# Optimization experiments

Hardware: AMD Instinct MI355X
Metric: run time of the kernel (lower is better)

The kernel has to match this reference:

```python
import jax, jax.numpy as jnp
import numpy as np

B, S, D = 2, 2048, 2048
H, KV, HD = 32, 8, 64          # n_heads, n_kv_heads, head_dim
REP = H // KV                  # 4
THETA = 10000.0


def _rotate_half(u):
    h = u.shape[-1] // 2
    return jnp.concatenate([-u[..., h:], u[..., :h]], axis=-1)


def setup_inputs() -> dict:
    key = jax.random.key(0)
    ks = jax.random.split(key, 5)
    x = jax.random.normal(ks[0], (B, S, D), dtype=jnp.float32)
    Wq = jax.random.normal(ks[1], (D, H * HD), dtype=jnp.float32) * 0.02
    Wk = jax.random.normal(ks[2], (D, KV * HD), dtype=jnp.float32) * 0.02
    Wv = jax.random.normal(ks[3], (D, KV * HD), dtype=jnp.float32) * 0.02
    Wo = jax.random.normal(ks[4], (H * HD, D), dtype=jnp.float32) * 0.02
    return {"x": x, "Wq": Wq, "Wk": Wk, "Wv": Wv, "Wo": Wo}


def reference(x, Wq, Wk, Wv, Wo):
    b, s, d = x.shape
    # QKV projections (nn.Linear, no bias)
    q = (x @ Wq).reshape(b, s, H, HD).transpose(0, 2, 1, 3)   # [B,H,S,HD]
    k = (x @ Wk).reshape(b, s, KV, HD).transpose(0, 2, 1, 3)  # [B,KV,S,HD]
    v = (x @ Wv).reshape(b, s, KV, HD).transpose(0, 2, 1, 3)  # [B,KV,S,HD]

    # RoPE (position_offset = 0)
    inv_freq = 1.0 / (THETA ** (jnp.arange(0, HD, 2, dtype=jnp.float32) / HD))
    freqs = jnp.outer(jnp.arange(s, dtype=jnp.float32), inv_freq)  # [S,HD/2]
    emb = jnp.concatenate([freqs, freqs], axis=-1)                  # [S,HD]
    cos, sin = jnp.cos(emb), jnp.sin(emb)
    q = q * cos + _rotate_half(q) * sin
    k = k * cos + _rotate_half(k) * sin

    # Grouped attention: avoid materializing repeated KV tensors.
    qg = q.reshape(b, KV, REP, s, HD)                               # [B,KV,REP,S,HD]
    scale = 1.0 / np.sqrt(HD)
    scores = jnp.einsum('bgrqd,bgkd->bgrqk', qg, k) * scale         # [B,KV,REP,S,S]
    causal = jnp.tril(jnp.ones((s, s), dtype=bool))
    scores = jnp.where(causal, scores, jnp.finfo(jnp.float32).min)
    probs = jax.nn.softmax(scores.astype(jnp.float32), axis=-1).astype(q.dtype)
    out = jnp.einsum('bgrqk,bgkd->bgrqd', probs, v)                 # [B,KV,REP,S,HD]
    out = out.reshape(b, H, s, HD).transpose(0, 2, 1, 3).reshape(b, s, H * HD)
    return out @ Wo                                                  # [B,S,D]
```

## Files before the change

kernel.cpp:

```cpp
#include <hip/hip_runtime.h>
#include <math.h>

typedef __bf16 bf16_t;
typedef bf16_t bf16x8 __attribute__((ext_vector_type(8)));
typedef bf16_t bf16x4 __attribute__((ext_vector_type(4)));
typedef float floatx4 __attribute__((ext_vector_type(4)));
typedef short short4v __attribute__((ext_vector_type(4)));

#define MFMA16(a, b, c) __builtin_amdgcn_mfma_f32_16x16x32_bf16((a), (b), (c), 0, 0, 0)

#if __has_builtin(__builtin_amdgcn_exp2f)
#define PEXP(x) __builtin_amdgcn_exp2f(x)
#define SCORE_SCALE (0.125f * 1.4426950408889634f)
#else
#define PEXP(x) __expf(x)
#define SCORE_SCALE 0.125f
#endif

#if __has_builtin(__builtin_amdgcn_mfma_f32_16x16x16bf16_1k)
#define HAVE_MFMA_K16 1
__device__ __forceinline__ floatx4 mfma_k16(bf16x4 a, bf16x4 b, floatx4 c)
{
    union { bf16x4 v; short4v s; } ua, ub;
    ua.v = a; ub.v = b;
    return __builtin_amdgcn_mfma_f32_16x16x16bf16_1k(ua.s, ub.s, c, 0, 0, 0);
}
#endif

union PU { unsigned u[2]; bf16x4 v; };
union BU { unsigned u[4]; bf16x8 v; };

__device__ __forceinline__ void gld16(const void* g, void* lds)
{
    __builtin_amdgcn_global_load_lds(
        reinterpret_cast<const __attribute__((address_space(1))) void*>(
            reinterpret_cast<uintptr_t>(g)),
        reinterpret_cast<__attribute__((address_space(3))) void*>(
            (unsigned int)reinterpret_cast<uintptr_t>(lds)),
        16, 0, 0);
}

template <typename TC>
__device__ __forceinline__ void gemm_bt_body(
    const bf16_t* __restrict__ A, const bf16_t* __restrict__ Bt,
    TC* __restrict__ C, int row0, int col0, int N, int K,
    bf16_t* As, bf16_t* Bs)
{
    const int tid  = threadIdx.x;
    const int wave = tid >> 6, lane = tid & 63;
    const int quad = lane >> 4, l16 = lane & 15;
    const int wm = (wave >> 1) * 64, wn = (wave & 1) * 64;

    floatx4 acc[4][4] = {};

    for (int k0 = 0; k0 < K; k0 += 64) {
        __syncthreads();
        #pragma unroll
        for (int i = 0; i < 4; ++i) {
            int c = i * 256 + tid;
            int r = c >> 3, s = c & 7;
            int ks = k0 + ((s ^ (r & 7)) << 3);
            gld16(A  + (size_t)(row0 + r) * K + ks, &As[(i * 256 + wave * 64) * 8]);
            gld16(Bt + (size_t)(col0 + r) * K + ks, &Bs[(i * 256 + wave * 64) * 8]);
        }
        __syncthreads();
        #pragma unroll
        for (int kh = 0; kh < 2; ++kh) {
            bf16x8 af[4], bfr[4];
            #pragma unroll
            for (int t = 0; t < 4; ++t) {
                int ar = wm + t * 16 + l16;
                af[t]  = *(const bf16x8*)&As[ar * 64 + (((kh * 4 + quad) ^ (ar & 7)) << 3)];
                int br = wn + t * 16 + l16;
                bfr[t] = *(const bf16x8*)&Bs[br * 64 + (((kh * 4 + quad) ^ (br & 7)) << 3)];
            }
            #pragma unroll
            for (int mt = 0; mt < 4; ++mt)
                #pragma unroll
                for (int nt = 0; nt < 4; ++nt)
                    acc[mt][nt] = MFMA16(af[mt], bfr[nt], acc[mt][nt]);
        }
    }
    #pragma unroll
    for (int mt = 0; mt < 4; ++mt)
        #pragma unroll
        for (int nt = 0; nt < 4; ++nt)
            #pragma unroll
            for (int r = 0; r < 4; ++r)
                C[(size_t)(row0 + wm + mt * 16 + quad * 4 + r) * N
                  + col0 + wn + nt * 16 + l16] = (TC)acc[mt][nt][r];
}

template <typename TC>
__global__ __launch_bounds__(256) void gemm_bt(
    const bf16_t* __restrict__ A, const bf16_t* __restrict__ Bt,
    TC* __restrict__ C, int N, int K)
{
    __shared__ bf16_t As[128 * 64];
    __shared__ bf16_t Bs[128 * 64];
    gemm_bt_body<TC>(A, Bt, C, blockIdx.y * 128, blockIdx.x * 128, N, K, As, Bs);
}

__global__ __launch_bounds__(256) void gemm_qkv(
    const bf16_t* __restrict__ A, const bf16_t* __restrict__ BtQ,
    const bf16_t* __restrict__ BtK, const bf16_t* __restrict__ BtV,
    bf16_t* __restrict__ CQ, bf16_t* __restrict__ CK, bf16_t* __restrict__ CV)
{
    __shared__ bf16_t As[128 * 64];
    __shared__ bf16_t Bs[128 * 64];
    const int x = blockIdx.x;
    const bf16_t* Bt; bf16_t* C; int N, col0;
    if (x < 16)      { Bt = BtQ; C = CQ; N = 2048; col0 = x * 128; }
    else if (x < 20) { Bt = BtK; C = CK; N = 512;  col0 = (x - 16) * 128; }
    else             { Bt = BtV; C = CV; N = 512;  col0 = (x - 20) * 128; }
    gemm_bt_body<bf16_t>(A, Bt, C, blockIdx.y * 128, col0, N, 2048, As, Bs);
}

__device__ __forceinline__ void transpose_body(
    const float* __restrict__ W, bf16_t* __restrict__ Wt, int K, int N,
    int bx, int by, float (*t)[33], int tid)
{
    int tx = tid & 31, ty = tid >> 5;
    #pragma unroll
    for (int i = 0; i < 32; i += 8)
        t[ty + i][tx] = W[(size_t)(by + ty + i) * N + bx + tx];
    __syncthreads();
    #pragma unroll
    for (int i = 0; i < 32; i += 8)
        Wt[(size_t)(bx + ty + i) * K + by + tx] = (bf16_t)t[tx][ty + i];
}

__global__ __launch_bounds__(256) void prep_all(
    const float* __restrict__ x, const float* __restrict__ Wq,
    const float* __restrict__ Wk, const float* __restrict__ Wv,
    bf16_t* __restrict__ xb, bf16_t* __restrict__ WqT,
    bf16_t* __restrict__ WkT, bf16_t* __restrict__ WvT)
{
    __shared__ float t[32][33];
    const int blk = blockIdx.x, tid = threadIdx.x;
    if (blk < 8192) {
        int i = blk * 256 + tid;
        float4 f = ((const float4*)x)[i];
        bf16x4 v = {(bf16_t)f.x, (bf16_t)f.y, (bf16_t)f.z, (bf16_t)f.w};
        ((bf16x4*)xb)[i] = v;
    } else if (blk < 12288) {
        int r = blk - 8192;
        transpose_body(Wq, WqT, 2048, 2048, (r & 63) * 32, (r >> 6) * 32, t, tid);
    } else if (blk < 13312) {
        int r = blk - 12288;
        transpose_body(Wk, WkT, 2048, 512, (r & 15) * 32, (r >> 4) * 32, t, tid);
    } else {
        int r = blk - 13312;
        transpose_body(Wv, WvT, 2048, 512, (r & 15) * 32, (r >> 4) * 32, t, tid);
    }
}

__global__ __launch_bounds__(256) void mid_all(
    bf16_t* __restrict__ Kw, const bf16_t* __restrict__ Vw,
    bf16_t* __restrict__ VtG, const float* __restrict__ Wo,
    bf16_t* __restrict__ WoT)
{
    __shared__ float tf[32][33];
    __shared__ bf16_t tb[32][34];
    const int blk = blockIdx.x, tid = threadIdx.x;
    if (blk < 4096) {
        int idx = blk * 256 + tid;
        int i   = idx & 31;
        int h   = (idx >> 5) & 7;
        int row = idx >> 8;
        int pos = row & 2047;
        float invf = powf(10000.0f, -(float)i / 32.0f);
        float sv, cv;
        sincosf((float)pos * invf, &sv, &cv);
        size_t base = (size_t)row * 512 + (size_t)h * 64 + i;
        float a  = (float)Kw[base];
        float b2 = (float)Kw[base + 32];
        Kw[base]      = (bf16_t)(a * cv - b2 * sv);
        Kw[base + 32] = (bf16_t)(b2 * cv + a * sv);
    } else if (blk < 6144) {
        int r  = blk - 4096;
        int bz = r >> 10, r2 = r & 1023;
        int bx = (r2 & 15) * 32, by = (r2 >> 4) * 32;
        int tx = tid & 31, ty = tid >> 5;
        #pragma unroll
        for (int i = 0; i < 32; i += 8)
            tb[ty + i][tx] = Vw[((size_t)bz * 2048 + by + ty + i) * 512 + bx + tx];
        __syncthreads();
        #pragma unroll
        for (int i = 0; i < 32; i += 8)
            VtG[((size_t)bz * 512 + bx + ty + i) * 2048 + by + tx] = tb[tx][ty + i];
    } else {
        int r = blk - 6144;
        transpose_body(Wo, WoT, 2048, 2048, (r & 63) * 32, (r >> 6) * 32, tf, tid);
    }
}

__global__ __launch_bounds__(256) void gqa_attn(
    const bf16_t* __restrict__ Q, const bf16_t* __restrict__ Kc,
    const bf16_t* __restrict__ Vt, bf16_t* __restrict__ AO)
{
    __shared__ alignas(16) bf16_t Ks[2][64 * 64];
    __shared__ alignas(16) bf16_t Vs[2][64 * 64];

    const int x = blockIdx.x, h = blockIdx.y, b = blockIdx.z, g = h >> 2;
    const int tid  = threadIdx.x;
    const int wave = tid >> 6, lane = tid & 63;
    const int quad = lane >> 4, l16 = lane & 15;

    #pragma unroll 1
    for (int t = 0; t < 2; ++t) {
        const int qt = t ? x : (15 - x);
        const int q0 = qt * 128;
        int qb[2];
        qb[0] = q0 + wave * 16;
        qb[1] = qb[0] + 64;

        bf16x8 qf[2][2];
        #pragma unroll
        for (int mt = 0; mt < 2; ++mt) {
            int qrow = qb[mt] + l16;
            const bf16_t* qp = Q + (size_t)(b * 2048 + qrow) * 2048 + h * 64 + quad * 8;
            bf16x8 lo = *(const bf16x8*)qp;
            bf16x8 hi = *(const bf16x8*)(qp + 32);
            #pragma unroll
            for (int j = 0; j < 8; ++j) {
                int d = quad * 8 + j;
                float invf = powf(10000.0f, -(float)d / 32.0f);
                float sv, cv;
                sincosf((float)qrow * invf, &sv, &cv);
                float a = (float)lo[j], c2 = (float)hi[j];
                qf[mt][0][j] = (bf16_t)((a * cv - c2 * sv) * SCORE_SCALE);
                qf[mt][1][j] = (bf16_t)((c2 * cv + a * sv) * SCORE_SCALE);
            }
        }

        floatx4 o[2][4] = {};
        floatx4 ls4[2] = {};

        const int ktmax = 2 * qt + 1;

        __asm__ volatile("s_waitcnt lgkmcnt(0)" ::: "memory");
        __builtin_amdgcn_s_barrier();
        #pragma unroll
        for (int i = 0; i < 2; ++i) {
            int c = i * 256 + tid;
            int r = c >> 3, s = c & 7;
            int sw = (s ^ (r & 7)) << 3;
            gld16(Kc + (size_t)(b * 2048 + r) * 512 + g * 64 + sw,
                  &Ks[0][(i * 256 + wave * 64) * 8]);
            gld16(Vt + (size_t)(b * 512 + g * 64 + r) * 2048 + sw,
                  &Vs[0][(i * 256 + wave * 64) * 8]);
        }

        #pragma unroll 1
        for (int kt = 0; kt <= ktmax; ++kt) {
            const int cur = kt & 1;
            if (kt < ktmax) {
                const int kn = kt + 1;
                #pragma unroll
                for (int i = 0; i < 2; ++i) {
                    int c = i * 256 + tid;
                    int r = c >> 3, s = c & 7;
                    int sw = (s ^ (r & 7)) << 3;
                    gld16(Kc + (size_t)(b * 2048 + kn * 64 + r) * 512 + g * 64 + sw,
                          &Ks[cur ^ 1][(i * 256 + wave * 64) * 8]);
                    gld16(Vt + (size_t)(b * 512 + g * 64 + r) * 2048 + kn * 64 + sw,
                          &Vs[cur ^ 1][(i * 256 + wave * 64) * 8]);
                }
                __asm__ volatile("s_waitcnt vmcnt(4)" ::: "memory");
            } else {
                __asm__ volatile("s_waitcnt vmcnt(0)" ::: "memory");
            }
            __builtin_amdgcn_s_barrier();

            bool en[2];
            en[0] = (kt * 64) <= (qb[0] + 15);
            en[1] = (kt * 64) <= (qb[1] + 15);

            floatx4 st[2][4] = {};
            #pragma unroll
            for (int nt = 0; nt < 4; ++nt) {
                int kr = nt * 16 + l16;
                bf16x8 kf0 = *(const bf16x8*)&Ks[cur][kr * 64 + ((quad ^ (kr & 7)) << 3)];
                bf16x8 kf1 = *(const bf16x8*)&Ks[cur][kr * 64 + (((4 + quad) ^ (kr & 7)) << 3)];
                if (en[0]) {
                    st[0][nt] = MFMA16(kf0, qf[0][0], st[0][nt]);
                    st[0][nt] = MFMA16(kf1, qf[0][1], st[0][nt]);
                }
                if (en[1]) {
                    st[1][nt] = MFMA16(kf0, qf[1][0], st[1][nt]);
                    st[1][nt] = MFMA16(kf1, qf[1][1], st[1][nt]);
                }
            }

            PU pk[2][4];
            #pragma unroll
            for (int mt = 0; mt < 2; ++mt) {
                if (!en[mt]) continue;
                const bool diag = (kt * 64 + 63) > qb[mt];
                const int qa = qb[mt] + l16;
                #pragma unroll
                for (int nt = 0; nt < 4; ++nt) {
                    float pv[4];
                    #pragma unroll
                    for (int r = 0; r < 4; ++r) {
                        float e = PEXP(st[mt][nt][r]);
                        if (diag) {
                            int ka = kt * 64 + nt * 16 + quad * 4 + r;
                            if (ka > qa) e = 0.f;
                        }
                        ls4[mt][r] += e;
                        pv[r] = e;
                    }
                    pk[mt][nt].v = bf16x4{(bf16_t)pv[0], (bf16_t)pv[1],
                                          (bf16_t)pv[2], (bf16_t)pv[3]};
                }
            }

#ifdef HAVE_MFMA_K16
            #pragma unroll
            for (int nt = 0; nt < 4; ++nt)
                #pragma unroll
                for (int dt = 0; dt < 4; ++dt) {
                    int vr = dt * 16 + l16;
                    int slot = ((nt << 1) | (quad >> 1)) ^ (vr & 7);
                    bf16x4 va = *(const bf16x4*)&Vs[cur][vr * 64 + (slot << 3)
                                                         + ((quad & 1) << 2)];
                    if (en[0]) o[0][dt] = mfma_k16(va, pk[0][nt].v, o[0][dt]);
                    if (en[1]) o[1][dt] = mfma_k16(va, pk[1][nt].v, o[1][dt]);
                }
#else
            #pragma unroll
            for (int H = 0; H < 2; ++H) {
                BU bfv[2];
                #pragma unroll
                for (int mt = 0; mt < 2; ++mt) {
                    if (!en[mt]) continue;
                    #pragma unroll
                    for (int j = 0; j < 4; ++j) {
                        int srcl = (((quad & 1) << 1) + (j >> 1)) * 16 + l16;
                        unsigned a0 = (unsigned)__shfl((int)pk[mt][2 * H].u[j & 1], srcl, 64);
                        unsigned a1 = (unsigned)__shfl((int)pk[mt][2 * H + 1].u[j & 1], srcl, 64);
                        bfv[mt].u[j] = (quad >> 1) ? a1 : a0;
                    }
                }
                #pragma unroll
                for (int dt = 0; dt < 4; ++dt) {
                    int vr = dt * 16 + l16;
                    bf16x8 va = *(const bf16x8*)&Vs[cur][vr * 64
                                  + ((((H << 2) | quad) ^ (vr & 7)) << 3)];
                    if (en[0]) o[0][dt] = MFMA16(va, bfv[0].v, o[0][dt]);
                    if (en[1]) o[1][dt] = MFMA16(va, bfv[1].v, o[1][dt]);
                }
            }
#endif
            __asm__ volatile("s_waitcnt lgkmcnt(0)" ::: "memory");
            __builtin_amdgcn_s_barrier();
        }

        #pragma unroll
        for (int mt = 0; mt < 2; ++mt) {
            float l = ls4[mt][0] + ls4[mt][1] + ls4[mt][2] + ls4[mt][3];
            l += __shfl_xor(l, 16, 64);
            l += __shfl_xor(l, 32, 64);
            float rc = 1.0f / l;
            #pragma unroll
            for (int dt = 0; dt < 4; ++dt) {
                bf16x4 ov = {(bf16_t)(o[mt][dt][0] * rc), (bf16_t)(o[mt][dt][1] * rc),
                             (bf16_t)(o[mt][dt][2] * rc), (bf16_t)(o[mt][dt][3] * rc)};
                *(bf16x4*)&AO[(size_t)(b * 2048 + qb[mt] + l16) * 2048
                              + h * 64 + dt * 16 + quad * 4] = ov;
            }
        }
    }
}

extern "C" void kernel_launch(void* const* d_in, const int* in_sizes, int n_in,
                              void* d_out, int out_size, void* d_ws, size_t ws_size,
                              hipStream_t stream)
{
    const float* x  = (const float*)d_in[0];
    const float* Wq = (const float*)d_in[1];
    const float* Wk = (const float*)d_in[2];
    const float* Wv = (const float*)d_in[3];
    const float* Wo = (const float*)d_in[4];
    float* out = (float*)d_out;

    const size_t MB = 1024 * 1024;
    char* ws = (char*)d_ws;
    bf16_t* xb_AO = (bf16_t*)(ws);
    bf16_t* WqoT  = (bf16_t*)(ws + 16 * MB);
    bf16_t* WkT   = (bf16_t*)(ws + 24 * MB);
    bf16_t* WvT   = (bf16_t*)(ws + 26 * MB);
    bf16_t* Qw    = (bf16_t*)(ws + 28 * MB);
    bf16_t* Kw    = (bf16_t*)(ws + 44 * MB);
    bf16_t* Vw    = (bf16_t*)(ws + 48 * MB);
    bf16_t* VtG   = (bf16_t*)(ws + 52 * MB);

    prep_all<<<14336, 256, 0, stream>>>(x, Wq, Wk, Wv, xb_AO, WqoT, WkT, WvT);

    gemm_qkv<<<dim3(24, 32), 256, 0, stream>>>(xb_AO, WqoT, WkT, WvT, Qw, Kw, Vw);

    mid_all<<<10240, 256, 0, stream>>>(Kw, Vw, VtG, Wo, WqoT);

    gqa_attn<<<dim3(8, 32, 2), 256, 0, stream>>>(Qw, Kw, VtG, xb_AO);

    gemm_bt<float><<<dim3(16, 32), 256, 0, stream>>>(xb_AO, WqoT, out, 2048, 2048);
}
```

Measured before the change: 327.5 us.

## Move Q RoPE into mid kernel and halve attention query tile to 64 rows

Q RoPE and score scaling move out of the attention kernel into new blocks of mid_all, so each Q element is rotated once in a separate pass instead of inside the attention prologue. The attention kernel now handles 64 query rows per tile instead of 128, doubling the grid. It also skips fully masked 16-column subtiles on the diagonal block. The extra elementwise pass costs one read and one write of Q, and smaller tiles mean K/V tiles are loaded twice as often per query row.

Measured after the change: 330.8 us. About the same (+1.0%).

```diff
diff --git a/kernel.cpp b/kernel.cpp
--- a/kernel.cpp
+++ b/kernel.cpp
@@ -158,7 +158,7 @@
 __global__ __launch_bounds__(256) void mid_all(
     bf16_t* __restrict__ Kw, const bf16_t* __restrict__ Vw,
     bf16_t* __restrict__ VtG, const float* __restrict__ Wo,
-    bf16_t* __restrict__ WoT)
+    bf16_t* __restrict__ WoT, bf16_t* __restrict__ Qw)
 {
     __shared__ float tf[32][33];
     __shared__ bf16_t tb[32][34];
@@ -168,10 +168,9 @@
         int i   = idx & 31;
         int h   = (idx >> 5) & 7;
         int row = idx >> 8;
-        int pos = row & 2047;
         float invf = powf(10000.0f, -(float)i / 32.0f);
         float sv, cv;
-        sincosf((float)pos * invf, &sv, &cv);
+        sincosf((float)(row & 2047) * invf, &sv, &cv);
         size_t base = (size_t)row * 512 + (size_t)h * 64 + i;
         float a  = (float)Kw[base];
         float b2 = (float)Kw[base + 32];
@@ -189,9 +188,22 @@
         #pragma unroll
         for (int i = 0; i < 32; i += 8)
             VtG[((size_t)bz * 512 + bx + ty + i) * 2048 + by + tx] = tb[tx][ty + i];
-    } else {
+    } else if (blk < 10240) {
         int r = blk - 6144;
         transpose_body(Wo, WoT, 2048, 2048, (r & 63) * 32, (r >> 6) * 32, tf, tid);
+    } else {
+        int idx = (blk - 10240) * 256 + tid;
+        int i   = idx & 31;
+        int h   = (idx >> 5) & 31;
+        int row = idx >> 10;
+        float invf = powf(10000.0f, -(float)i / 32.0f);
+        float sv, cv;
+        sincosf((float)(row & 2047) * invf, &sv, &cv);
+        size_t base = (size_t)row * 2048 + (size_t)h * 64 + i;
+        float a  = (float)Qw[base];
+        float b2 = (float)Qw[base + 32];
+        Qw[base]      = (bf16_t)((a * cv - b2 * sv) * SCORE_SCALE);
+        Qw[base + 32] = (bf16_t)((b2 * cv + a * sv) * SCORE_SCALE);
     }
 }
 
@@ -209,38 +221,18 @@
 
     #pragma unroll 1
     for (int t = 0; t < 2; ++t) {
-        const int qt = t ? x : (15 - x);
-        const int q0 = qt * 128;
-        int qb[2];
-        qb[0] = q0 + wave * 16;
-        qb[1] = qb[0] + 64;
-
-        bf16x8 qf[2][2];
-        #pragma unroll
-        for (int mt = 0; mt < 2; ++mt) {
-            int qrow = qb[mt] + l16;
-            const bf16_t* qp = Q + (size_t)(b * 2048 + qrow) * 2048 + h * 64 + quad * 8;
-            bf16x8 lo = *(const bf16x8*)qp;
-            bf16x8 hi = *(const bf16x8*)(qp + 32);
-            #pragma unroll
-            for (int j = 0; j < 8; ++j) {
-                int d = quad * 8 + j;
-                float invf = powf(10000.0f, -(float)d / 32.0f);
-                float sv, cv;
-                sincosf((float)qrow * invf, &sv, &cv);
-                float a = (float)lo[j], c2 = (float)hi[j];
-                qf[mt][0][j] = (bf16_t)((a * cv - c2 * sv) * SCORE_SCALE);
-                qf[mt][1][j] = (bf16_t)((c2 * cv + a * sv) * SCORE_SCALE);
-            }
-        }
-
-        floatx4 o[2][4] = {};
-        floatx4 ls4[2] = {};
-
-        const int ktmax = 2 * qt + 1;
-
-        __asm__ volatile("s_waitcnt lgkmcnt(0)" ::: "memory");
-        __builtin_amdgcn_s_barrier();
+        const int qt = t ? x : (31 - x);
+        const int qb = qt * 64 + wave * 16;
+
+        const bf16_t* qp = Q + (size_t)(b * 2048 + qb + l16) * 2048 + h * 64 + quad * 8;
+        bf16x8 qf0 = *(const bf16x8*)qp;
+        bf16x8 qf1 = *(const bf16x8*)(qp + 32);
+
+        floatx4 o[4] = {};
+        floatx4 ls4 = {};
+
+        const int ktmax = qt;
+
         #pragma unroll
         for (int i = 0; i < 2; ++i) {
             int c = i * 256 + tid;
@@ -273,84 +265,70 @@
             }
             __builtin_amdgcn_s_barrier();
 
-            bool en[2];
-            en[0] = (kt * 64) <= (qb[0] + 15);
-            en[1] = (kt * 64) <= (qb[1] + 15);
-
-            floatx4 st[2][4] = {};
+            floatx4 st[4] = {};
             #pragma unroll
             for (int nt = 0; nt < 4; ++nt) {
                 int kr = nt * 16 + l16;
                 bf16x8 kf0 = *(const bf16x8*)&Ks[cur][kr * 64 + ((quad ^ (kr & 7)) << 3)];
                 bf16x8 kf1 = *(const bf16x8*)&Ks[cur][kr * 64 + (((4 + quad) ^ (kr & 7)) << 3)];
-                if (en[0]) {
-                    st[0][nt] = MFMA16(kf0, qf[0][0], st[0][nt]);
-                    st[0][nt] = MFMA16(kf1, qf[0][1], st[0][nt]);
-                }
-                if (en[1]) {
-                    st[1][nt] = MFMA16(kf0, qf[1][0], st[1][nt]);
-                    st[1][nt] = MFMA16(kf1, qf[1][1], st[1][nt]);
-                }
-            }
-
-            PU pk[2][4];
-            #pragma unroll
-            for (int mt = 0; mt < 2; ++mt) {
-                if (!en[mt]) continue;
-                const bool diag = (kt * 64 + 63) > qb[mt];
-                const int qa = qb[mt] + l16;
-                #pragma unroll
-                for (int nt = 0; nt < 4; ++nt) {
+                st[nt] = MFMA16(kf0, qf0, st[nt]);
+                st[nt] = MFMA16(kf1, qf1, st[nt]);
+            }
+
+            const bool diag = (kt == qt);
+            const int ntlim = diag ? wave : 3;
+
+            PU pk[4];
+            #pragma unroll
+            for (int nt = 0; nt < 4; ++nt) {
+                if (nt <= ntlim) {
                     float pv[4];
                     #pragma unroll
                     for (int r = 0; r < 4; ++r) {
-                        float e = PEXP(st[mt][nt][r]);
-                        if (diag) {
-                            int ka = kt * 64 + nt * 16 + quad * 4 + r;
-                            if (ka > qa) e = 0.f;
+                        float e = PEXP(st[nt][r]);
+                        if (diag && nt == wave) {
+                            if (quad * 4 + r > l16) e = 0.f;
                         }
-                        ls4[mt][r] += e;
+                        ls4[r] += e;
                         pv[r] = e;
                     }
-                    pk[mt][nt].v = bf16x4{(bf16_t)pv[0], (bf16_t)pv[1],
-                                          (bf16_t)pv[2], (bf16_t)pv[3]};
+                    pk[nt].v = bf16x4{(bf16_t)pv[0], (bf16_t)pv[1],
+                                      (bf16_t)pv[2], (bf16_t)pv[3]};
+                } else {
+                    pk[nt].u[0] = 0; pk[nt].u[1] = 0;
                 }
             }
 
 #ifdef HAVE_MFMA_K16
             #pragma unroll
-            for (int nt = 0; nt < 4; ++nt)
+            for (int nt = 0; nt < 4; ++nt) {
+                if (nt > ntlim) continue;
                 #pragma unroll
                 for (int dt = 0; dt < 4; ++dt) {
                     int vr = dt * 16 + l16;
                     int slot = ((nt << 1) | (quad >> 1)) ^ (vr & 7);
                     bf16x4 va = *(const bf16x4*)&Vs[cur][vr * 64 + (slot << 3)
                                                          + ((quad & 1) << 2)];
-                    if (en[0]) o[0][dt] = mfma_k16(va, pk[0][nt].v, o[0][dt]);
-                    if (en[1]) o[1][dt] = mfma_k16(va, pk[1][nt].v, o[1][dt]);
-                }
+                    o[dt] = mfma_k16(va, pk[nt].v, o[dt]);
+                }
+            }
 #else
             #pragma unroll
             for (int H = 0; H < 2; ++H) {
-                BU bfv[2];
-                #pragma unroll
-                for (int mt = 0; mt < 2; ++mt) {
-                    if (!en[mt]) continue;
-                    #pragma unroll
-                    for (int j = 0; j < 4; ++j) {
-                        int srcl = (((quad & 1) << 1) + (j >> 1)) * 16 + l16;
-                        unsigned a0 = (unsigned)__shfl((int)pk[mt][2 * H].u[j & 1], srcl, 64);
-                        unsigned a1 = (unsigned)__shfl((int)pk[mt][2 * H + 1].u[j & 1], srcl, 64);
-                        bfv[mt].u[j] = (quad >> 1) ? a1 : a0;
-                    }
+                BU bfv;
+                #pragma unroll
+                for (int j = 0; j < 4; ++j) {
+                    int srcl = (((quad & 1) << 1) + (j >> 1)) * 16 + l16;
+                    unsigned a0 = (unsigned)__shfl((int)pk[2 * H].u[j & 1], srcl, 64);
+                    unsigned a1 = (unsigned)__shfl((int)pk[2 * H + 1].u[j & 1], srcl, 64);
+                    bfv.u[j] = (quad >> 1) ? a1 : a0;
                 }
                 #pragma unroll
                 for (int dt = 0; dt < 4; ++dt) {
                     int vr = dt * 16 + l16;
                     bf16x8 va = *(const bf16x8*)&Vs[cur][vr * 64
                                   + ((((H << 2) | quad) ^ (vr & 7)) << 3)];
-                    if (en[0]) o[0][dt] = MFMA16(va, bfv[0].v, o[0][dt]);
-                    if (en[1]) o[1][dt] = MFMA16(va, bfv[1].v, o[1][dt]);
+                    o[dt] = MFMA16(va, bfv.v, o[dt]);
                 }
             }
 #endif
@@ -358,19 +336,16 @@
             __builtin_amdgcn_s_barrier();
         }
 
-        #pragma unroll
-        for (int mt = 0; mt < 2; ++mt) {
-            float l = ls4[mt][0] + ls4[mt][1] + ls4[mt][2] + ls4[mt][3];
-            l += __shfl_xor(l, 16, 64);
-            l += __shfl_xor(l, 32, 64);
-            float rc = 1.0f / l;
-            #pragma unroll
-            for (int dt = 0; dt < 4; ++dt) {
-                bf16x4 ov = {(bf16_t)(o[mt][dt][0] * rc), (bf16_t)(o[mt][dt][1] * rc),
-                             (bf16_t)(o[mt][dt][2] * rc), (bf16_t)(o[mt][dt][3] * rc)};
-                *(bf16x4*)&AO[(size_t)(b * 2048 + qb[mt] + l16) * 2048
-                              + h * 64 + dt * 16 + quad * 4] = ov;
-            }
+        float l = ls4[0] + ls4[1] + ls4[2] + ls4[3];
+        l += __shfl_xor(l, 16, 64);
+        l += __shfl_xor(l, 32, 64);
+        float rc = 1.0f / l;
+        #pragma unroll
+        for (int dt = 0; dt < 4; ++dt) {
+            bf16x4 ov = {(bf16_t)(o[dt][0] * rc), (bf16_t)(o[dt][1] * rc),
+                         (bf16_t)(o[dt][2] * rc), (bf16_t)(o[dt][3] * rc)};
+            *(bf16x4*)&AO[(size_t)(b * 2048 + qb + l16) * 2048
+                          + h * 64 + dt * 16 + quad * 4] = ov;
         }
     }
 }
@@ -401,9 +376,9 @@
 
     gemm_qkv<<<dim3(24, 32), 256, 0, stream>>>(xb_AO, WqoT, WkT, WvT, Qw, Kw, Vw);
 
-    mid_all<<<10240, 256, 0, stream>>>(Kw, Vw, VtG, Wo, WqoT);
-
-    gqa_attn<<<dim3(8, 32, 2), 256, 0, stream>>>(Qw, Kw, VtG, xb_AO);
+    mid_all<<<26624, 256, 0, stream>>>(Kw, Vw, VtG, Wo, WqoT, Qw);
+
+    gqa_attn<<<dim3(16, 32, 2), 256, 0, stream>>>(Qw, Kw, VtG, xb_AO);
 
     gemm_bt<float><<<dim3(16, 32), 256, 0, stream>>>(xb_AO, WqoT, out, 2048, 2048);
 }
```
